# Kernel tuning notes

Measured on AMD Instinct MI355X. Metric: run time of the kernel, lower is better.

## Reference

```python
import jax, jax.numpy as jnp
import numpy as np

EMBEDDING_DIM = 256
NUM_EMBEDDINGS = 8192
COMMITMENT_COST = 0.25
DECAY = 0.99
EPSILON = 1e-5


def setup_inputs() -> dict:
    key = jax.random.key(0)
    k1, k2 = jax.random.split(key)
    inputs = jax.random.normal(k1, (16, 32, 32, EMBEDDING_DIM), dtype=jnp.float32)
    # VarianceScaling(distribution='uniform'), fan_in scaling over [D, K]
    limit = float(np.sqrt(3.0 / EMBEDDING_DIM))
    embeddings = jax.random.uniform(k2, (EMBEDDING_DIM, NUM_EMBEDDINGS),
                                    minval=-limit, maxval=limit, dtype=jnp.float32)
    return {
        'inputs': inputs,
        'embeddings': embeddings,
        'ema_cs_hidden': jnp.zeros((NUM_EMBEDDINGS,), jnp.float32),
        'ema_dw_hidden': embeddings,  # hk initializes ema_dw to the embeddings
        'counter': 0,
        'is_training': 1,
    }


def reference(inputs, embeddings, ema_cs_hidden, ema_dw_hidden, counter, is_training):
    flat = inputs.reshape(-1, EMBEDDING_DIM)                        # [N, D]
    distances = (jnp.sum(flat ** 2, axis=1, keepdims=True)
                 - 2.0 * (flat @ embeddings)
                 + jnp.sum(embeddings ** 2, axis=0, keepdims=True))  # [N, K]
    encoding_indices = jnp.argmax(-distances, axis=1)                # [N]
    encodings = jax.nn.one_hot(encoding_indices, NUM_EMBEDDINGS,
                               dtype=distances.dtype)                # [N, K]
    idx = encoding_indices.reshape(inputs.shape[:-1])
    quantized = embeddings.T[idx]                                    # gather codebook
    e_latent_loss = jnp.mean((jax.lax.stop_gradient(quantized) - inputs) ** 2)
    loss = COMMITMENT_COST * e_latent_loss

    if is_training:
        # haiku ExponentialMovingAverage with zero-debias
        new_counter = counter + 1
        debias = 1.0 - DECAY ** new_counter
        cs_hidden = ema_cs_hidden * DECAY + jnp.sum(encodings, axis=0) * (1.0 - DECAY)
        cs_avg = cs_hidden / debias                                  # [K]
        dw = flat.T @ encodings                                      # [D, K] scatter-add as GEMM
        dw_hidden = ema_dw_hidden * DECAY + dw * (1.0 - DECAY)
        dw_avg = dw_hidden / debias
        n = jnp.sum(cs_avg)
        cs_norm = (cs_avg + EPSILON) / (n + NUM_EMBEDDINGS * EPSILON) * n
        new_embeddings = dw_avg / cs_norm[None, :]                   # [D, K]
    else:
        new_embeddings = embeddings

    # straight-through estimator
    quantized_st = inputs + jax.lax.stop_gradient(quantized - inputs)
    avg_probs = jnp.mean(encodings, axis=0)
    perplexity = jnp.exp(-jnp.sum(avg_probs * jnp.log(avg_probs + 1e-10)))
    return (quantized_st, loss, perplexity, idx, new_embeddings)
```

## Files before the change

### kernel.cpp

```cpp
#include <hip/hip_runtime.h>
#include <math.h>

#define DD 256
#define KK 8192
#define NN 16384
#define DECAYF 0.99f
#define EPSF 1e-5f
#define TAU 4e-3f

#define O_Q    0
#define O_LOSS 4194304
#define O_PERP 4194305
#define O_IDX  4194306
#define O_EMB  4210690

typedef float f32x4 __attribute__((ext_vector_type(4)));
typedef _Float16 f16x8 __attribute__((ext_vector_type(8)));

__device__ __forceinline__ unsigned short f2h(float f) {
  union { _Float16 h; unsigned short u; } c;
  c.h = (_Float16)f;
  return c.u;
}

__device__ __forceinline__ void gll16(const void* g, void* l) {
  __builtin_amdgcn_global_load_lds((const __attribute__((address_space(1))) void*)g,
                                   (__attribute__((address_space(3))) void*)l, 16, 0, 0);
}

__global__ void k_convert_xe(const float* __restrict__ x, unsigned short* __restrict__ Ah,
                             const float* __restrict__ emb, unsigned short* __restrict__ Eh,
                             float* __restrict__ embT, float* __restrict__ esq) {
  __shared__ float ld[32 * 33];
  int bx = blockIdx.x;
  int t = threadIdx.x;
  if (bx < 4096) {
    int i = bx * 256 + t;
    float4 v = ((const float4*)x)[i];
    ushort4 h;
    h.x = f2h(v.x); h.y = f2h(v.y); h.z = f2h(v.z); h.w = f2h(v.w);
    ((ushort4*)Ah)[i] = h;
    return;
  }
  int eb = bx - 4096;
  int k0 = (eb & 255) * 32, d0 = (eb >> 8) * 32;
  {
    int din = t >> 3, kq = (t & 7) * 4;
    float4 v = *(const float4*)(emb + (size_t)(d0 + din) * KK + k0 + kq);
    ld[din * 33 + kq + 0] = v.x; ld[din * 33 + kq + 1] = v.y;
    ld[din * 33 + kq + 2] = v.z; ld[din * 33 + kq + 3] = v.w;
  }
  __syncthreads();
  int kout = t >> 3, dq = (t & 7) * 4;
  float f0 = ld[(dq + 0) * 33 + kout], f1 = ld[(dq + 1) * 33 + kout];
  float f2 = ld[(dq + 2) * 33 + kout], f3 = ld[(dq + 3) * 33 + kout];
  size_t o = (size_t)(k0 + kout) * DD + d0 + dq;
  float4 fv; fv.x = f0; fv.y = f1; fv.z = f2; fv.w = f3;
  *(float4*)(embT + o) = fv;
  ushort4 hv;
  hv.x = f2h(f0); hv.y = f2h(f1); hv.z = f2h(f2); hv.w = f2h(f3);
  *(ushort4*)(Eh + o) = hv;
  float p = (f0 * f0 + f1 * f1) + (f2 * f2 + f3 * f3);
  p += __shfl_xor(p, 1, 64);
  p += __shfl_xor(p, 2, 64);
  p += __shfl_xor(p, 4, 64);
  if ((t & 7) == 0) atomicAdd(esq + k0 + kout, p);
}

__launch_bounds__(256, 2)
__global__ void k_dist_mfma(const unsigned short* __restrict__ Ah, const unsigned short* __restrict__ Bh,
                            const float* __restrict__ esq,
                            float* __restrict__ part1, float* __restrict__ part2,
                            int* __restrict__ partidx) {
  __shared__ __align__(16) unsigned short sB[8192];

  const int tid = threadIdx.x;
  const int w = tid >> 6, lane = tid & 63;
  const int kb = blockIdx.x, nb = blockIdx.y;
  const int row0 = nb * 128, col0 = kb * 128;
  const int m = lane & 15, q = lane >> 4;

  size_t gB[4];
  int lbB[4];
  #pragma unroll
  for (int s = 0; s < 4; ++s) {
    int g = w * 4 + s;
    int r = g * 8 + (lane >> 3);
    int c = (lane & 7) ^ (r & 7);
    gB[s] = (size_t)(col0 + r) * DD + c * 8;
    lbB[s] = g * 512;
  }

  const unsigned short* pA0 = Ah + (size_t)(row0 + w * 32 + m) * DD + q * 8;
  const unsigned short* pA1 = pA0 + 16 * DD;

  f32x4 acc[2][8];
  #pragma unroll
  for (int i = 0; i < 2; ++i)
    #pragma unroll
    for (int j = 0; j < 8; ++j) acc[i][j] = (f32x4)0.f;

  for (int it = 0; it < 4; ++it) {
    const int d0 = it * 64;
    __syncthreads();
    #pragma unroll
    for (int s = 0; s < 4; ++s) gll16(Bh + gB[s] + d0, sB + lbB[s]);
    f16x8 a[2][2];
    #pragma unroll
    for (int kk = 0; kk < 2; ++kk) {
      a[kk][0] = *(const f16x8*)(pA0 + d0 + kk * 32);
      a[kk][1] = *(const f16x8*)(pA1 + d0 + kk * 32);
    }
    __syncthreads();
    #pragma unroll
    for (int kk = 0; kk < 2; ++kk) {
      #pragma unroll
      for (int j = 0; j < 8; ++j) {
        int cn = j * 16 + m;
        int slot = (kk * 4 + q) ^ (cn & 7);
        f16x8 b = *(const f16x8*)(sB + cn * 64 + slot * 8);
        acc[0][j] = __builtin_amdgcn_mfma_f32_16x16x32_f16(a[kk][0], b, acc[0][j], 0, 0, 0);
        acc[1][j] = __builtin_amdgcn_mfma_f32_16x16x32_f16(a[kk][1], b, acc[1][j], 0, 0, 0);
      }
    }
  }

  float eq[8];
  #pragma unroll
  for (int j = 0; j < 8; ++j) eq[j] = esq[col0 + j * 16 + m];

  #pragma unroll
  for (int i = 0; i < 2; ++i) {
    #pragma unroll
    for (int reg = 0; reg < 4; ++reg) {
      float m1 = 3.402823466e+38f, m2 = 3.402823466e+38f;
      int bi = 0;
      #pragma unroll
      for (int j = 0; j < 8; ++j) {
        float dd = fmaf(-2.0f, acc[i][j][reg], eq[j]);
        bool p = dd < m1;
        m2 = fminf(m2, fmaxf(dd, m1));
        m1 = fminf(m1, dd);
        bi = p ? (col0 + j * 16 + m) : bi;
      }
      #pragma unroll
      for (int st = 1; st < 16; st <<= 1) {
        float ov = __shfl_xor(m1, st, 64);
        int   oi = __shfl_xor(bi, st, 64);
        float o2 = __shfl_xor(m2, st, 64);
        m2 = fminf(fminf(m2, o2), fmaxf(m1, ov));
        bool p = ov < m1;
        m1 = fminf(m1, ov);
        bi = p ? oi : bi;
      }
      if (m == 0) {
        int prow = row0 + w * 32 + i * 16 + q * 4 + reg;
        int pidx = prow * 64 + kb;
        part1[pidx] = m1; part2[pidx] = m2; partidx[pidx] = bi;
      }
    }
  }
}

__global__ void k_argmin2(float* __restrict__ part1, float* __restrict__ part2,
                          const int* __restrict__ partidx, int* __restrict__ idxw,
                          int* __restrict__ listc, int* __restrict__ list) {
  int w = threadIdx.x >> 6, l = threadIdx.x & 63;
  int row = blockIdx.x * 4 + w;
  int f = blockIdx.x * 256 + threadIdx.x;
  float m1 = part1[f], m2 = part2[f];
  int bi = partidx[f];
  part1[f] = 0.f;
  part2[f] = 0.f;
  #pragma unroll
  for (int st = 1; st < 64; st <<= 1) {
    float ov = __shfl_xor(m1, st, 64);
    int   oi = __shfl_xor(bi, st, 64);
    float o2 = __shfl_xor(m2, st, 64);
    m2 = fminf(fminf(m2, o2), fmaxf(m1, ov));
    bool p = ov < m1;
    m1 = fminf(m1, ov);
    bi = p ? oi : bi;
  }
  if (l == 0) {
    idxw[row] = bi;
    if (m2 - m1 < TAU) { int pos = atomicAdd(listc, 1); list[pos] = row; }
  }
}

__global__ void k_rescore(const float* __restrict__ x, const float* __restrict__ emb,
                          const int* __restrict__ listc, const int* __restrict__ list,
                          unsigned long long* __restrict__ keys) {
  __shared__ float se[8192];
  __shared__ double red[256];
  const int t = threadIdx.x;
  const int k0 = blockIdx.x * 32;
  #pragma unroll
  for (int i = 0; i < 32; ++i) {
    int elem = i * 256 + t;
    int d = elem >> 5, c = elem & 31;
    se[d * 32 + c] = emb[(size_t)d * KK + k0 + c];
  }
  __syncthreads();
  const int c = t & 31, p = t >> 5;
  int cnt = *listc;
  for (int li = blockIdx.y; li < cnt; li += gridDim.y) {
    int row = list[li];
    const float* xr = x + (size_t)row * DD;
    double acc = 0.0;
    #pragma unroll
    for (int j = 0; j < 32; ++j) {
      int d = p * 32 + j;
      double df = (double)xr[d] - (double)se[d * 32 + c];
      acc = fma(df, df, acc);
    }
    red[c * 8 + p] = acc;
    __syncthreads();
    if (t < 64) {
      unsigned long long key = ~0ull;
      if (t < 32) {
        double dist = 0.0;
        #pragma unroll
        for (int qq = 0; qq < 8; ++qq) dist += red[t * 8 + qq];
        key = ((unsigned long long)__double_as_longlong(dist) & ~0x1FFFull)
              | (unsigned long long)(k0 + t);
      }
      #pragma unroll
      for (int s = 1; s < 64; s <<= 1) {
        unsigned long long o = __shfl_xor(key, s, 64);
        if (o < key) key = o;
      }
      if (t == 0) atomicMin(&keys[row], key);
    }
    __syncthreads();
  }
}

__global__ void k_gather(const float* __restrict__ x, const float* __restrict__ embT,
                         const int* __restrict__ idxw, const unsigned long long* __restrict__ keys,
                         const int* __restrict__ train,
                         float* __restrict__ outq, float* __restrict__ outidx,
                         float* __restrict__ dwT, float* __restrict__ counts,
                         float* __restrict__ loss_part) {
  int w = threadIdx.x >> 6, l = threadIdx.x & 63;
  int n = blockIdx.x * 4 + w;
  unsigned long long kv = keys[n];
  int k = (kv != ~0ull) ? (int)(kv & 0x1FFFull) : idxw[n];
  float4 xv = ((const float4*)(x + (size_t)n * DD))[l];
  float4 qv = ((const float4*)(embT + (size_t)k * DD))[l];
  int d = l * 4;

  ((float4*)(outq + (size_t)n * DD))[l] = qv;

  float e0 = qv.x - xv.x, e1 = qv.y - xv.y, e2 = qv.z - xv.z, e3 = qv.w - xv.w;
  float ls = (e0 * e0 + e1 * e1) + (e2 * e2 + e3 * e3);

  if (*train) {
    const float wdw = 1.0f - DECAYF;
    float* base = dwT + (size_t)k * DD + d;
    atomicAdd(base + 0, xv.x * wdw);
    atomicAdd(base + 1, xv.y * wdw);
    atomicAdd(base + 2, xv.z * wdw);
    atomicAdd(base + 3, xv.w * wdw);
  }

  #pragma unroll
  for (int s = 1; s < 64; s <<= 1) ls += __shfl_xor(ls, s, 64);
  if (l == 0) {
    atomicAdd(&loss_part[blockIdx.x & 255], ls);
    atomicAdd(&counts[k], 1.0f);
    outidx[n] = (float)k;
  }
}

__global__ void k_stats(const float* __restrict__ counts, const float* __restrict__ ema_cs,
                        const int* __restrict__ counter, const int* __restrict__ train,
                        const float* __restrict__ loss_part, float* __restrict__ csn,
                        float* __restrict__ outloss, float* __restrict__ outperp) {
  __shared__ float s_n[4], s_e[4], s_l[4], s_tot[1];
  int tid = threadIdx.x;
  float debias = 1.0f - powf(DECAYF, (float)(*counter + 1));
  float nloc = 0.f, eloc = 0.f;
  float lloc = loss_part[tid];
  float avg[32];
  for (int i = 0; i < 32; ++i) {
    int k = tid + i * 256;
    float c = counts[k];
    float h = ema_cs[k] * DECAYF + c * (1.0f - DECAYF);
    float a = h / debias;
    avg[i] = a;
    nloc += a;
    float p = c * (1.0f / 16384.0f);
    eloc += p * logf(p + 1e-10f);
  }
  #pragma unroll
  for (int s = 1; s < 64; s <<= 1) {
    nloc += __shfl_xor(nloc, s, 64);
    eloc += __shfl_xor(eloc, s, 64);
    lloc += __shfl_xor(lloc, s, 64);
  }
  int w = tid >> 6, lane = tid & 63;
  if (lane == 0) { s_n[w] = nloc; s_e[w] = eloc; s_l[w] = lloc; }
  __syncthreads();
  if (tid == 0) {
    float nt = (s_n[0] + s_n[1]) + (s_n[2] + s_n[3]);
    float et = (s_e[0] + s_e[1]) + (s_e[2] + s_e[3]);
    float lt = (s_l[0] + s_l[1]) + (s_l[2] + s_l[3]);
    s_tot[0] = nt;
    outperp[0] = expf(-et);
    outloss[0] = 0.25f * (lt / 4194304.0f);
  }
  __syncthreads();
  float nsum = s_tot[0];
  float denom = nsum + 8192.0f * EPSF;
  for (int i = 0; i < 32; ++i) {
    int k = tid + i * 256;
    csn[k] = (avg[i] + EPSF) / denom * nsum;
  }
}

__global__ void k_final(const float* __restrict__ dwT, const float* __restrict__ ema_dw,
                        const float* __restrict__ emb, const float* __restrict__ csn,
                        const int* __restrict__ counter, const int* __restrict__ train,
                        float* __restrict__ out4) {
  __shared__ float ld[32 * 33];
  int t = threadIdx.x;
  int k0 = blockIdx.x * 32, d0 = blockIdx.y * 32;
  if (*train) {
    {
      int ki = t >> 3, dq = (t & 7) * 4;
      float4 v = *(const float4*)(dwT + (size_t)(k0 + ki) * DD + d0 + dq);
      ld[ki * 33 + dq + 0] = v.x; ld[ki * 33 + dq + 1] = v.y;
      ld[ki * 33 + dq + 2] = v.z; ld[ki * 33 + dq + 3] = v.w;
    }
    __syncthreads();
    int dout = t >> 3, kq = (t & 7) * 4;
    size_t o = (size_t)(d0 + dout) * KK + k0 + kq;
    float4 e = *(const float4*)(ema_dw + o);
    float4 c = *(const float4*)(csn + k0 + kq);
    float inv = 1.0f / (1.0f - powf(DECAYF, (float)(*counter + 1)));
    float4 r;
    r.x = fmaf(e.x, DECAYF, ld[(kq + 0) * 33 + dout]) * inv / c.x;
    r.y = fmaf(e.y, DECAYF, ld[(kq + 1) * 33 + dout]) * inv / c.y;
    r.z = fmaf(e.z, DECAYF, ld[(kq + 2) * 33 + dout]) * inv / c.z;
    r.w = fmaf(e.w, DECAYF, ld[(kq + 3) * 33 + dout]) * inv / c.w;
    *(float4*)(out4 + o) = r;
  } else {
    int dout = t >> 3, kq = (t & 7) * 4;
    size_t o = (size_t)(d0 + dout) * KK + k0 + kq;
    *(float4*)(out4 + o) = *(const float4*)(emb + o);
  }
}

extern "C" void kernel_launch(void* const* d_in, const int* in_sizes, int n_in,
                              void* d_out, int out_size, void* d_ws, size_t ws_size,
                              hipStream_t stream) {
  (void)in_sizes; (void)n_in; (void)out_size; (void)ws_size;
  const float* x      = (const float*)d_in[0];
  const float* emb    = (const float*)d_in[1];
  const float* ema_cs = (const float*)d_in[2];
  const float* ema_dw = (const float*)d_in[3];
  const int*   counter = (const int*)d_in[4];
  const int*   train   = (const int*)d_in[5];

  float* out = (float*)d_out;
  float* outq    = out + O_Q;
  float* outloss = out + O_LOSS;
  float* outperp = out + O_PERP;
  float* outidx  = out + O_IDX;
  float* out4    = out + O_EMB;

  char* W = (char*)d_ws;
  unsigned short* Ah   = (unsigned short*)(W);
  unsigned short* Eh   = (unsigned short*)(W + 8388608);
  float* embT          = (float*)(W + 12582912);
  float* part1         = (float*)(W + 20971520);
  float* part2         = (float*)(W + 25165824);
  int*   partidx       = (int*)(W + 29360128);
  float* dwT           = part1;
  unsigned long long* keys = (unsigned long long*)(W + 33554432);
  float* esq           = (float*)(W + 33685504);
  float* csn           = (float*)(W + 33718272);
  float* counts        = (float*)(W + 33751040);
  float* loss_part     = (float*)(W + 33783808);
  int*   listc         = (int*)(W + 33784832);
  int*   list          = (int*)(W + 33784836);
  int*   idxw          = (int*)(W + 33850372);

  hipMemsetAsync(esq, 0, 99332, stream);
  hipMemsetAsync(keys, 0xFF, NN * sizeof(unsigned long long), stream);

  k_convert_xe<<<6144, 256, 0, stream>>>(x, Ah, emb, Eh, embT, esq);
  k_dist_mfma<<<dim3(64, 128), 256, 0, stream>>>(Ah, Eh, esq, part1, part2, partidx);
  k_argmin2<<<4096, 256, 0, stream>>>(part1, part2, partidx, idxw, listc, list);
  k_rescore<<<dim3(256, 8), 256, 0, stream>>>(x, emb, listc, list, keys);
  k_gather<<<4096, 256, 0, stream>>>(x, embT, idxw, keys, train, outq, outidx, dwT, counts, loss_part);
  k_stats<<<1, 256, 0, stream>>>(counts, ema_cs, counter, train, loss_part, csn, outloss, outperp);
  k_final<<<dim3(256, 8), 256, 0, stream>>>(dwT, ema_dw, emb, csn, counter, train, out4);
}
```

Measured before the change: 370.1 us.

## Double-buffer codebook tiles and prefetch A fragments in distance GEMM

Converts the distance MFMA kernel's K-loop to a double-buffered pipeline. The next 64-wide slice of B goes into the alternate LDS buffer and the next A fragments into registers while MFMAs run on the current slice. Manual vmcnt waits and raw s_barrier calls replace the two __syncthreads per iteration. This doubles LDS use (32KB per block) and adds register pressure under launch_bounds(256,2), and the hand-counted vmcnt is fragile if the compiler reorders loads.

```diff
diff --git a/kernel.cpp b/kernel.cpp
--- a/kernel.cpp
+++ b/kernel.cpp
@@ -72,7 +72,7 @@
                             const float* __restrict__ esq,
                             float* __restrict__ part1, float* __restrict__ part2,
                             int* __restrict__ partidx) {
-  __shared__ __align__(16) unsigned short sB[8192];
+  __shared__ __align__(16) unsigned short sB[2][8192];
 
   const int tid = threadIdx.x;
   const int w = tid >> 6, lane = tid & 63;
@@ -100,29 +100,46 @@
     #pragma unroll
     for (int j = 0; j < 8; ++j) acc[i][j] = (f32x4)0.f;
 
+  f16x8 aR[2][4];
+
+  #pragma unroll
+  for (int s = 0; s < 4; ++s) gll16(Bh + gB[s], sB[0] + lbB[s]);
+  aR[0][0] = *(const f16x8*)(pA0);
+  aR[0][1] = *(const f16x8*)(pA1);
+  aR[0][2] = *(const f16x8*)(pA0 + 32);
+  aR[0][3] = *(const f16x8*)(pA1 + 32);
+
+  #pragma unroll
   for (int it = 0; it < 4; ++it) {
-    const int d0 = it * 64;
-    __syncthreads();
-    #pragma unroll
-    for (int s = 0; s < 4; ++s) gll16(Bh + gB[s] + d0, sB + lbB[s]);
-    f16x8 a[2][2];
-    #pragma unroll
-    for (int kk = 0; kk < 2; ++kk) {
-      a[kk][0] = *(const f16x8*)(pA0 + d0 + kk * 32);
-      a[kk][1] = *(const f16x8*)(pA1 + d0 + kk * 32);
-    }
-    __syncthreads();
+    if (it < 3) {
+      const int d1 = (it + 1) * 64;
+      unsigned short* dst = sB[(it + 1) & 1];
+      #pragma unroll
+      for (int s = 0; s < 4; ++s) gll16(Bh + gB[s] + d1, dst + lbB[s]);
+      f16x8* an = aR[(it + 1) & 1];
+      an[0] = *(const f16x8*)(pA0 + d1);
+      an[1] = *(const f16x8*)(pA1 + d1);
+      an[2] = *(const f16x8*)(pA0 + d1 + 32);
+      an[3] = *(const f16x8*)(pA1 + d1 + 32);
+      asm volatile("s_waitcnt vmcnt(8)" ::: "memory");
+    } else {
+      asm volatile("s_waitcnt vmcnt(0)" ::: "memory");
+    }
+    __builtin_amdgcn_s_barrier();
+    const unsigned short* sb = sB[it & 1];
+    const f16x8* ac = aR[it & 1];
     #pragma unroll
     for (int kk = 0; kk < 2; ++kk) {
       #pragma unroll
       for (int j = 0; j < 8; ++j) {
         int cn = j * 16 + m;
         int slot = (kk * 4 + q) ^ (cn & 7);
-        f16x8 b = *(const f16x8*)(sB + cn * 64 + slot * 8);
-        acc[0][j] = __builtin_amdgcn_mfma_f32_16x16x32_f16(a[kk][0], b, acc[0][j], 0, 0, 0);
-        acc[1][j] = __builtin_amdgcn_mfma_f32_16x16x32_f16(a[kk][1], b, acc[1][j], 0, 0, 0);
-      }
-    }
+        f16x8 b = *(const f16x8*)(sb + cn * 64 + slot * 8);
+        acc[0][j] = __builtin_amdgcn_mfma_f32_16x16x32_f16(ac[kk * 2 + 0], b, acc[0][j], 0, 0, 0);
+        acc[1][j] = __builtin_amdgcn_mfma_f32_16x16x32_f16(ac[kk * 2 + 1], b, acc[1][j], 0, 0, 0);
+      }
+    }
+    if (it < 3) __builtin_amdgcn_s_barrier();
   }
 
   float eq[8];
```

Result: no change. 372.2 us (+0.6%).
